# Kernel optimization log

Hardware: AMD Instinct MI355X
Metric: run time of the kernel (lower is better)

The kernel has to match this reference:

```python
import jax, jax.numpy as jnp
import numpy as np

B, S, D, H = 2, 2048, 1024, 16
DK = D // H  # 64


def setup_inputs() -> dict:
    key = jax.random.key(0)
    ks = jax.random.split(key, 12)
    inp = {
        "q": jax.random.normal(ks[0], (B, S, D), jnp.float32),
        "k": jax.random.normal(ks[1], (B, S, D), jnp.float32),
        "v": jax.random.normal(ks[2], (B, S, D), jnp.float32),
        "mask": jax.random.randint(ks[3], (B, S, S), 0, 2).astype(bool),
        "prior_info": jax.random.normal(ks[4], (B, S, S), jnp.float32),
        # per-head q/k projections stacked [H, D, DK]; shared v projection [D, DK]
        "Wq": jax.random.normal(ks[5], (H, D, DK), jnp.float32) * 0.02,
        "bq": jnp.zeros((H, DK), jnp.float32),
        "Wk": jax.random.normal(ks[6], (H, D, DK), jnp.float32) * 0.02,
        "bk": jnp.zeros((H, DK), jnp.float32),
        "Wv": jax.random.normal(ks[7], (D, DK), jnp.float32) * 0.02,
        "bv": jnp.zeros((DK,), jnp.float32),
        "Wh": jax.random.normal(ks[8], (DK, D), jnp.float32) * 0.02,  # w_h, no bias
    }
    return inp


def reference(q, k, v, mask, prior_info, Wq, bq, Wk, bk, Wv, bv, Wh):
    NEG = jnp.asarray(-1e9, q.dtype)
    vs = v @ Wv + bv                                      # [B,S,DK] shared across heads
    qs = jnp.einsum("bsd,hdk->bhsk", q, Wq) + bq[None, :, None, :]
    ksh = jnp.einsum("btd,hdk->bhtk", k, Wk) + bk[None, :, None, :]
    scores = jnp.einsum("bhsk,bhtk->bhst", qs, ksh) / jnp.sqrt(
        jnp.asarray(DK, q.dtype))                         # [B,H,S,S]
    m = mask[:, None]                                     # [B,1,S,S]
    scores = jnp.where(m, NEG, scores)
    prior = jnp.where(m, NEG, prior_info[:, None])        # [B,1,S,S] -> broadcast
    z = jax.nn.sigmoid(scores + prior)
    blended = z * scores + (1 - z) * prior
    attn = jax.nn.softmax(blended, axis=-1)               # [B,H,S,S]
    heads = jnp.einsum("bhst,btk->bhsk", attn, vs)        # [B,H,S,DK]
    out = heads.mean(axis=1) @ Wh                          # [B,S,D]
    attn_out = jnp.transpose(attn, (0, 2, 1, 3))           # torch stacks heads at dim=2
    return out, attn_out
```

## Files before the change

kernel.cpp:

```cpp
#include <hip/hip_runtime.h>

#define DEV __device__ __forceinline__

using f32x4  = __attribute__((ext_vector_type(4))) float;
using bf16x8 = __attribute__((ext_vector_type(8))) __bf16;
using u16x4  = __attribute__((ext_vector_type(4))) unsigned short;

constexpr int S_ = 2048, D_ = 1024, H_ = 16, DK_ = 64;
constexpr float LOG2E_ = 1.44269504f;
constexpr float M2_ = 8.0f * 1.44269504f;
constexpr float C1_ = 0.125f * 1.44269504f;

DEV unsigned short f2bf(float x) {
  unsigned int u = __float_as_uint(x);
  u += 0x7fffu + ((u >> 16) & 1u);
  return (unsigned short)(u >> 16);
}

DEV float bf2f(unsigned short u) {
  return __uint_as_float((unsigned int)u << 16);
}

DEV void gload_lds16(const void* g, void* l) {
  __builtin_amdgcn_global_load_lds(
      (__attribute__((address_space(1))) void*)g,
      (__attribute__((address_space(3))) void*)l, 16, 0, 0);
}

DEV f32x4 mfma_bf16(bf16x8 a, bf16x8 b, f32x4 c) {
  return __builtin_amdgcn_mfma_f32_16x16x32_bf16(a, b, c, 0, 0, 0);
}


__global__ __launch_bounds__(256) void qkv_to_bf16(
    const float* __restrict__ q, const float* __restrict__ k,
    const float* __restrict__ v, unsigned short* __restrict__ dst) {
  int seg = blockIdx.x >> 12;
  int j = ((blockIdx.x & 4095) << 8) + threadIdx.x;
  const float* s = seg == 0 ? q : (seg == 1 ? k : v);
  unsigned short* d = dst + (size_t)seg * 4194304;
  f32x4 val = *(const f32x4*)(s + (size_t)j * 4);
  u16x4 o;
  o[0] = f2bf(val[0]); o[1] = f2bf(val[1]); o[2] = f2bf(val[2]); o[3] = f2bf(val[3]);
  *(u16x4*)(d + (size_t)j * 4) = o;
}

__global__ __launch_bounds__(256) void make_pm2(
    const int* __restrict__ mask, const float* __restrict__ prior,
    unsigned short* __restrict__ pm2, int n4) {
  int i = blockIdx.x * 256 + threadIdx.x;
  if (i >= n4) return;
  const int* m = mask + (size_t)i * 4;
  f32x4 p = *(const f32x4*)(prior + (size_t)i * 4);
  u16x4 o;
#pragma unroll
  for (int j = 0; j < 4; ++j)
    o[j] = f2bf(m[j] ? -1.44269504e9f : p[j] * LOG2E_);
  *(u16x4*)(pm2 + (size_t)i * 4) = o;
}

__global__ __launch_bounds__(256) void pack_wqk2(
    const float* __restrict__ Wq, const float* __restrict__ Wk,
    unsigned short* __restrict__ WT) {
  int seg = blockIdx.x >> 12;
  int i = ((blockIdx.x & 4095) << 8) + threadIdx.x;
  const float* W = seg ? Wk : Wq;
  int d = i & 1023, n = i >> 10;
  int hh = n >> 6, kk = n & 63;
  WT[(size_t)seg * 1048576 + i] = f2bf(W[((size_t)hh * 1024 + d) * 64 + kk]);
}

__global__ __launch_bounds__(256) void pack_wv(
    const float* __restrict__ W, unsigned short* __restrict__ WT) {
  int i = blockIdx.x * 256 + threadIdx.x;
  int d = i & 1023, kk = i >> 10;
  WT[i] = f2bf(W[(size_t)d * 64 + kk]);
}

__global__ __launch_bounds__(256) void pack_wh(
    const float* __restrict__ W, unsigned short* __restrict__ WT) {
  int i = blockIdx.x * 256 + threadIdx.x;
  int k = i & 63, n = i >> 6;
  WT[i] = f2bf(W[(size_t)k * 1024 + n]);
}

__global__ __launch_bounds__(256) void mean_heads(
    const float* __restrict__ hp, unsigned short* __restrict__ hbar) {
  int i = blockIdx.x * 256 + threadIdx.x;
  int kk = i & 63, m = i >> 6;
  int b = m >> 11, s = m & 2047;
  float acc = 0.f;
#pragma unroll
  for (int hh = 0; hh < 16; ++hh)
    acc += hp[(((size_t)b * 16 + hh) * 2048 + s) * 64 + kk];
  hbar[i] = f2bf(acc * 0.0625f);
}


template <int BN, int MODE>
__global__ __launch_bounds__(256) void gemm_bt(
    const unsigned short* __restrict__ A, const unsigned short* __restrict__ BT,
    const float* __restrict__ bias, void* __restrict__ outp, int M, int N, int K) {
  constexpr int BM = 128, BK = 64;
  constexpr int NWC = BN / 64;
  constexpr int NWR = 4 / NWC;
  constexpr int WTM = BM / NWR;
  constexpr int MI = WTM / 16;
  constexpr int NI = 4;
  __shared__ unsigned short ldsA[BM * BK];
  __shared__ unsigned short ldsB[BN * BK];
  const int tid = threadIdx.x;
  const int wave = tid >> 6, lane = tid & 63;
  const int g = lane >> 4, l4 = lane & 15;
  const int m0 = blockIdx.x * BM, n0 = blockIdx.y * BN;
  const int wr = wave / NWC, wc = wave % NWC;
  const int r8 = lane >> 3, s8 = lane & 7;
  f32x4 acc[MI][NI];
#pragma unroll
  for (int mi = 0; mi < MI; ++mi)
#pragma unroll
    for (int ni = 0; ni < NI; ++ni) acc[mi][ni] = {0.f, 0.f, 0.f, 0.f};

  for (int k0 = 0; k0 < K; k0 += BK) {
    __syncthreads();
#pragma unroll
    for (int j = 0; j < 4; ++j) {
      int c = wave * 4 + j;
      int row = c * 8 + r8;
      int slot = s8 ^ (row & 7);
      gload_lds16(A + (size_t)(m0 + row) * K + k0 + slot * 8, &ldsA[c * 512]);
    }
    constexpr int BCH = BN * BK / 512;
#pragma unroll
    for (int j = 0; j < BCH / 4; ++j) {
      int c = wave * (BCH / 4) + j;
      int row = c * 8 + r8;
      int slot = s8 ^ (row & 7);
      gload_lds16(BT + (size_t)(n0 + row) * K + k0 + slot * 8, &ldsB[c * 512]);
    }
    __syncthreads();
    bf16x8 af[MI][2], bfr[NI][2];
#pragma unroll
    for (int mi = 0; mi < MI; ++mi)
#pragma unroll
      for (int kss = 0; kss < 2; ++kss) {
        int row = wr * WTM + mi * 16 + l4;
        int slot = (kss * 4 + g) ^ (row & 7);
        af[mi][kss] = *(const bf16x8*)&ldsA[row * 64 + slot * 8];
      }
#pragma unroll
    for (int ni = 0; ni < NI; ++ni)
#pragma unroll
      for (int kss = 0; kss < 2; ++kss) {
        int row = wc * 64 + ni * 16 + l4;
        int slot = (kss * 4 + g) ^ (row & 7);
        bfr[ni][kss] = *(const bf16x8*)&ldsB[row * 64 + slot * 8];
      }
#pragma unroll
    for (int mi = 0; mi < MI; ++mi)
#pragma unroll
      for (int ni = 0; ni < NI; ++ni)
#pragma unroll
        for (int kss = 0; kss < 2; ++kss)
          acc[mi][ni] = mfma_bf16(af[mi][kss], bfr[ni][kss], acc[mi][ni]);
  }

#pragma unroll
  for (int mi = 0; mi < MI; ++mi)
#pragma unroll
    for (int ni = 0; ni < NI; ++ni)
#pragma unroll
      for (int r = 0; r < 4; ++r) {
        int m = m0 + wr * WTM + mi * 16 + g * 4 + r;
        int n = n0 + wc * 64 + ni * 16 + l4;
        float c = acc[mi][ni][r];
        if constexpr (MODE != 2) c += bias[n];
        if constexpr (MODE == 0) {
          int b = m >> 11, s = m & 2047, hh = n >> 6, kk = n & 63;
          ((unsigned short*)outp)[(((size_t)b * 16 + hh) * 2048 + s) * 64 + kk] = f2bf(c);
        } else if constexpr (MODE == 1) {
          int b = m >> 11, t = m & 2047;
          ((unsigned short*)outp)[((size_t)b * 64 + n) * 2048 + t] = f2bf(c);
        } else {
          ((float*)outp)[(size_t)m * N + n] = c;
        }
      }
}


__global__ __launch_bounds__(512, 2) void attn_fused1(
    const unsigned short* __restrict__ qs, const unsigned short* __restrict__ ks,
    const unsigned short* __restrict__ vsT, const unsigned short* __restrict__ pm2,
    float* __restrict__ attn_out, float* __restrict__ heads) {
  __shared__ unsigned short lds_p[8][32 * 256];
  __shared__ float lds_sum[8][32];

  const int tid = threadIdx.x;
  const int w = tid >> 6, lane = tid & 63;
  const int g = lane >> 4, l4 = lane & 15;
  const int blk = ((blockIdx.x & 7) << 8) + (blockIdx.x >> 3);
  const int sblk = blk & 63, bh = blk >> 6;
  const int b = bh >> 4, h = bh & 15;
  const int tb = w << 8;

  const unsigned short* qsb = qs + ((size_t)bh * S_ + sblk * 32) * DK_;
  const unsigned short* ksb = ks + (size_t)bh * S_ * DK_ + (size_t)tb * DK_;
  const unsigned short* pmrow0 = pm2 + ((size_t)b * S_ + sblk * 32 + l4) * S_ + tb;
  const unsigned short* pmrow1 = pmrow0 + (size_t)16 * S_;
  const unsigned short* vtb = vsT + (size_t)b * DK_ * S_ + tb;

  bf16x8 aq0[2], aq1[2];
#pragma unroll
  for (int kss = 0; kss < 2; ++kss) {
    aq0[kss] = *(const bf16x8*)(qsb + (size_t)l4 * DK_ + (kss * 4 + g) * 8);
    aq1[kss] = *(const bf16x8*)(qsb + (size_t)(16 + l4) * DK_ + (kss * 4 + g) * 8);
  }

  char* pbase = (char*)&lds_p[w][0];
  const int swz = (l4 & 7) << 4;

  float lsum0 = 0.f, lsum1 = 0.f;
  u16x4 pc0[2][4], pc1[2][4];
#pragma unroll
  for (int d = 0; d < 2; ++d)
#pragma unroll
    for (int ct = 0; ct < 4; ++ct) {
      pc0[d][ct] = *(const u16x4*)(pmrow0 + d * 64 + ct * 16 + g * 4);
      pc1[d][ct] = *(const u16x4*)(pmrow1 + d * 64 + ct * 16 + g * 4);
    }
  bf16x8 kf[2][4][2];
#pragma unroll
  for (int ct = 0; ct < 4; ++ct)
#pragma unroll
    for (int kss = 0; kss < 2; ++kss)
      kf[0][ct][kss] = *(const bf16x8*)(ksb +
          (size_t)(ct * 16 + l4) * DK_ + (kss * 4 + g) * 8);

#pragma unroll
  for (int i = 0; i < 4; ++i) {
    const int tr = i * 64;
    const int cur = i & 1, nxt = (i + 1) & 1;
    if (i + 1 < 4) {
#pragma unroll
      for (int ct = 0; ct < 4; ++ct)
#pragma unroll
        for (int kss = 0; kss < 2; ++kss)
          kf[nxt][ct][kss] = *(const bf16x8*)(ksb +
              (size_t)((i + 1) * 64 + ct * 16 + l4) * DK_ + (kss * 4 + g) * 8);
    }
#pragma unroll
    for (int ct = 0; ct < 4; ++ct) {
      f32x4 a0 = {0.f, 0.f, 0.f, 0.f}, a1 = {0.f, 0.f, 0.f, 0.f};
#pragma unroll
      for (int kss = 0; kss < 2; ++kss) {
        a0 = mfma_bf16(kf[cur][ct][kss], aq0[kss], a0);
        a1 = mfma_bf16(kf[cur][ct][kss], aq1[kss], a1);
      }
      u16x4 pb0, pb1;
#pragma unroll
      for (int r = 0; r < 4; ++r) {
        {
          float pmv = bf2f(pc0[cur][ct][r]);
          float sc2 = a0[r] * C1_;
          float e = __builtin_amdgcn_exp2f(-(sc2 + pmv));
          float z = __builtin_amdgcn_rcpf(1.f + e);
          float p = __builtin_amdgcn_exp2f(pmv + z * (sc2 - pmv) - M2_);
          lsum0 += p;
          pb0[r] = f2bf(p);
        }
        {
          float pmv = bf2f(pc1[cur][ct][r]);
          float sc2 = a1[r] * C1_;
          float e = __builtin_amdgcn_exp2f(-(sc2 + pmv));
          float z = __builtin_amdgcn_rcpf(1.f + e);
          float p = __builtin_amdgcn_exp2f(pmv + z * (sc2 - pmv) - M2_);
          lsum1 += p;
          pb1[r] = f2bf(p);
        }
      }
      const int toff = ((tr + ct * 16 + g * 4) * 2) ^ swz;
      *(u16x4*)(pbase + (size_t)l4 * 512 + toff) = pb0;
      *(u16x4*)(pbase + (size_t)(16 + l4) * 512 + toff) = pb1;
    }
    if (i + 2 < 4) {
#pragma unroll
      for (int ct = 0; ct < 4; ++ct) {
        pc0[cur][ct] = *(const u16x4*)(pmrow0 + (i + 2) * 64 + ct * 16 + g * 4);
        pc1[cur][ct] = *(const u16x4*)(pmrow1 + (i + 2) * 64 + ct * 16 + g * 4);
      }
    }
  }
  lsum0 += __shfl_xor(lsum0, 16);
  lsum0 += __shfl_xor(lsum0, 32);
  lsum1 += __shfl_xor(lsum1, 16);
  lsum1 += __shfl_xor(lsum1, 32);
  if (g == 0) {
    lds_sum[w][l4] = lsum0;
    lds_sum[w][16 + l4] = lsum1;
  }

  __syncthreads();

  float invl0, invl1;
  {
    float s0 = 0.f, s1 = 0.f;
#pragma unroll
    for (int wv = 0; wv < 8; ++wv) {
      s0 += lds_sum[wv][l4];
      s1 += lds_sum[wv][16 + l4];
    }
    invl0 = 1.f / s0;
    invl1 = 1.f / s1;
  }

  f32x4 acc0_[4], acc1_[4];
#pragma unroll
  for (int ni = 0; ni < 4; ++ni) {
    acc0_[ni] = {0.f, 0.f, 0.f, 0.f};
    acc1_[ni] = {0.f, 0.f, 0.f, 0.f};
  }

  float* attrow0 = attn_out +
      (((size_t)b * S_ + sblk * 32 + l4) * H_ + h) * S_ + tb;
  float* attrow1 = attrow0 + (size_t)16 * H_ * S_;

  bf16x8 vf[2][4];
#pragma unroll
  for (int ni = 0; ni < 4; ++ni)
    vf[0][ni] = *(const bf16x8*)(vtb + (size_t)(ni * 16 + l4) * S_ + g * 8);

#pragma unroll
  for (int st = 0; st < 8; ++st) {
    const int t0 = st * 32;
    const int cur = st & 1, nxt = (st + 1) & 1;
    if (st + 1 < 8) {
#pragma unroll
      for (int ni = 0; ni < 4; ++ni)
        vf[nxt][ni] = *(const bf16x8*)(vtb +
            (size_t)(ni * 16 + l4) * S_ + t0 + 32 + g * 8);
    }
    const int toff = ((t0 + g * 8) * 2) ^ swz;
    bf16x8 pa0 = *(const bf16x8*)(pbase + (size_t)l4 * 512 + toff);
    bf16x8 pa1 = *(const bf16x8*)(pbase + (size_t)(16 + l4) * 512 + toff);
    f32x4 a0, a1, a2, a3;
#pragma unroll
    for (int j = 0; j < 4; ++j) {
      a0[j] = (float)pa0[j] * invl0;
      a1[j] = (float)pa0[4 + j] * invl0;
      a2[j] = (float)pa1[j] * invl1;
      a3[j] = (float)pa1[4 + j] * invl1;
    }
    *(f32x4*)(attrow0 + t0 + g * 8) = a0;
    *(f32x4*)(attrow0 + t0 + g * 8 + 4) = a1;
    *(f32x4*)(attrow1 + t0 + g * 8) = a2;
    *(f32x4*)(attrow1 + t0 + g * 8 + 4) = a3;
#pragma unroll
    for (int ni = 0; ni < 4; ++ni) {
      acc0_[ni] = mfma_bf16(pa0, vf[cur][ni], acc0_[ni]);
      acc1_[ni] = mfma_bf16(pa1, vf[cur][ni], acc1_[ni]);
    }
  }

  float* pr_lds = (float*)pbase;
#pragma unroll
  for (int ni = 0; ni < 4; ++ni)
#pragma unroll
    for (int r = 0; r < 4; ++r) {
      pr_lds[(g * 4 + r) * 64 + ni * 16 + l4] = acc0_[ni][r];
      pr_lds[(16 + g * 4 + r) * 64 + ni * 16 + l4] = acc1_[ni][r];
    }

  __syncthreads();

  {
    int row = tid >> 4;
    float sv = 0.f;
#pragma unroll
    for (int wv = 0; wv < 8; ++wv) sv += lds_sum[wv][row];
    float iv = 1.f / sv;
    f32x4 s4 = {0.f, 0.f, 0.f, 0.f};
#pragma unroll
    for (int wv = 0; wv < 8; ++wv) {
      f32x4 part = *(const f32x4*)((char*)&lds_p[wv][0] + tid * 16);
      s4[0] += part[0]; s4[1] += part[1]; s4[2] += part[2]; s4[3] += part[3];
    }
    s4[0] *= iv; s4[1] *= iv; s4[2] *= iv; s4[3] *= iv;
    *(f32x4*)(heads + ((size_t)bh * S_ + sblk * 32) * 64 + tid * 4) = s4;
  }
}


extern "C" void kernel_launch(void* const* d_in, const int* in_sizes, int n_in,
                              void* d_out, int out_size, void* d_ws, size_t ws_size,
                              hipStream_t stream) {
  (void)in_sizes; (void)n_in; (void)out_size; (void)ws_size;
  const float* q     = (const float*)d_in[0];
  const float* k     = (const float*)d_in[1];
  const float* v     = (const float*)d_in[2];
  const int*   mask  = (const int*)d_in[3];
  const float* prior = (const float*)d_in[4];
  const float* Wq    = (const float*)d_in[5];
  const float* bq    = (const float*)d_in[6];
  const float* Wk    = (const float*)d_in[7];
  const float* bk    = (const float*)d_in[8];
  const float* Wv    = (const float*)d_in[9];
  const float* bv    = (const float*)d_in[10];
  const float* Wh    = (const float*)d_in[11];

  float* out  = (float*)d_out;
  float* attn = out + (size_t)4096 * 1024;

  char* ws = (char*)d_ws;
  unsigned short* q_bf  = (unsigned short*)(ws + 0);
  unsigned short* pm2   = (unsigned short*)(ws + 0);
  float*          heads = (float*)(ws + 33554432);
  unsigned short* WqT   = (unsigned short*)(ws + 50331648);
  unsigned short* WvT   = (unsigned short*)(ws + 54525952);
  unsigned short* WhT   = (unsigned short*)(ws + 54657024);
  unsigned short* qs_bf = (unsigned short*)(ws + 54788096);
  unsigned short* ks_bf = (unsigned short*)(ws + 63176704);
  unsigned short* vsT   = (unsigned short*)(ws + 71565312);
  unsigned short* hbar  = (unsigned short*)(ws + 72089600);

  qkv_to_bf16<<<12288, 256, 0, stream>>>(q, k, v, q_bf);
  pack_wqk2<<<8192, 256, 0, stream>>>(Wq, Wk, WqT);
  pack_wv<<<256, 256, 0, stream>>>(Wv, WvT);
  pack_wh<<<256, 256, 0, stream>>>(Wh, WhT);

  gemm_bt<128, 0><<<dim3(32, 8), 256, 0, stream>>>(q_bf, WqT, bq, qs_bf, 4096, 1024, 1024);
  gemm_bt<128, 0><<<dim3(32, 8), 256, 0, stream>>>(q_bf + 4194304, WqT + 1048576, bk, ks_bf, 4096, 1024, 1024);
  gemm_bt<64, 1><<<dim3(32, 1), 256, 0, stream>>>(q_bf + 8388608, WvT, bv, vsT, 4096, 64, 1024);

  make_pm2<<<8192, 256, 0, stream>>>(mask, prior, pm2, 2097152);

  attn_fused1<<<2048, 512, 0, stream>>>(qs_bf, ks_bf, vsT, pm2, attn, heads);

  mean_heads<<<1024, 256, 0, stream>>>(heads, hbar);
  gemm_bt<128, 2><<<dim3(32, 8), 256, 0, stream>>>(hbar, WhT, nullptr, out, 4096, 1024, 64);
}
```

Measured before the change: 410.1 us.

## Pre-swizzle prior/mask tensor into per-wave fragment order and regroup heads per block

```diff
diff --git a/kernel.cpp b/kernel.cpp
--- a/kernel.cpp
+++ b/kernel.cpp
@@ -3,6 +3,7 @@
 #define DEV __device__ __forceinline__
 
 using f32x4  = __attribute__((ext_vector_type(4))) float;
+using int4v  = __attribute__((ext_vector_type(4))) int;
 using bf16x8 = __attribute__((ext_vector_type(8))) __bf16;
 using u16x4  = __attribute__((ext_vector_type(4))) unsigned short;
 
@@ -45,18 +46,24 @@
   *(u16x4*)(d + (size_t)j * 4) = o;
 }
 
-__global__ __launch_bounds__(256) void make_pm2(
+__global__ __launch_bounds__(256) void make_pm3(
     const int* __restrict__ mask, const float* __restrict__ prior,
-    unsigned short* __restrict__ pm2, int n4) {
-  int i = blockIdx.x * 256 + threadIdx.x;
-  if (i >= n4) return;
-  const int* m = mask + (size_t)i * 4;
-  f32x4 p = *(const f32x4*)(prior + (size_t)i * 4);
+    unsigned short* __restrict__ pm3) {
+  int tid = blockIdx.x * 256 + threadIdx.x;
+  int lane = tid & 63, cidx = tid >> 6;
+  int rs = cidx & 1, ct = (cidx >> 1) & 3, i = (cidx >> 3) & 3;
+  int w = (cidx >> 5) & 7, sblk = (cidx >> 8) & 63, b = cidx >> 14;
+  int g = lane >> 4, l4 = lane & 15;
+  int s = sblk * 32 + rs * 16 + l4;
+  int t = w * 256 + i * 64 + ct * 16 + g * 4;
+  size_t off = ((size_t)b * S_ + s) * S_ + t;
+  int4v m = *(const int4v*)(mask + off);
+  f32x4 p = *(const f32x4*)(prior + off);
   u16x4 o;
 #pragma unroll
   for (int j = 0; j < 4; ++j)
     o[j] = f2bf(m[j] ? -1.44269504e9f : p[j] * LOG2E_);
-  *(u16x4*)(pm2 + (size_t)i * 4) = o;
+  *(u16x4*)(pm3 + (size_t)tid * 4) = o;
 }
 
 __global__ __launch_bounds__(256) void pack_wqk2(
@@ -190,7 +197,7 @@
 
 __global__ __launch_bounds__(512, 2) void attn_fused1(
     const unsigned short* __restrict__ qs, const unsigned short* __restrict__ ks,
-    const unsigned short* __restrict__ vsT, const unsigned short* __restrict__ pm2,
+    const unsigned short* __restrict__ vsT, const unsigned short* __restrict__ pm3,
     float* __restrict__ attn_out, float* __restrict__ heads) {
   __shared__ unsigned short lds_p[8][32 * 256];
   __shared__ float lds_sum[8][32];
@@ -199,14 +206,16 @@
   const int w = tid >> 6, lane = tid & 63;
   const int g = lane >> 4, l4 = lane & 15;
   const int blk = ((blockIdx.x & 7) << 8) + (blockIdx.x >> 3);
-  const int sblk = blk & 63, bh = blk >> 6;
-  const int b = bh >> 4, h = bh & 15;
+  const int b = blk >> 10;
+  const int h = ((blk >> 9) & 1) * 8 + (blk & 7);
+  const int sblk = (blk >> 3) & 63;
+  const int bh = b * 16 + h;
   const int tb = w << 8;
 
   const unsigned short* qsb = qs + ((size_t)bh * S_ + sblk * 32) * DK_;
   const unsigned short* ksb = ks + (size_t)bh * S_ * DK_ + (size_t)tb * DK_;
-  const unsigned short* pmrow0 = pm2 + ((size_t)b * S_ + sblk * 32 + l4) * S_ + tb;
-  const unsigned short* pmrow1 = pmrow0 + (size_t)16 * S_;
+  const unsigned short* pmw = pm3 +
+      ((size_t)((b * 64 + sblk) * 8 + w) * 32) * 256;
   const unsigned short* vtb = vsT + (size_t)b * DK_ * S_ + tb;
 
   bf16x8 aq0[2], aq1[2];
@@ -225,8 +234,8 @@
   for (int d = 0; d < 2; ++d)
 #pragma unroll
     for (int ct = 0; ct < 4; ++ct) {
-      pc0[d][ct] = *(const u16x4*)(pmrow0 + d * 64 + ct * 16 + g * 4);
-      pc1[d][ct] = *(const u16x4*)(pmrow1 + d * 64 + ct * 16 + g * 4);
+      pc0[d][ct] = *(const u16x4*)(pmw + (size_t)((d * 4 + ct) * 2 + 0) * 256 + lane * 4);
+      pc1[d][ct] = *(const u16x4*)(pmw + (size_t)((d * 4 + ct) * 2 + 1) * 256 + lane * 4);
     }
   bf16x8 kf[2][4][2];
 #pragma unroll
@@ -285,8 +294,8 @@
     if (i + 2 < 4) {
 #pragma unroll
       for (int ct = 0; ct < 4; ++ct) {
-        pc0[cur][ct] = *(const u16x4*)(pmrow0 + (i + 2) * 64 + ct * 16 + g * 4);
-        pc1[cur][ct] = *(const u16x4*)(pmrow1 + (i + 2) * 64 + ct * 16 + g * 4);
+        pc0[cur][ct] = *(const u16x4*)(pmw + (size_t)(((i + 2) * 4 + ct) * 2 + 0) * 256 + lane * 4);
+        pc1[cur][ct] = *(const u16x4*)(pmw + (size_t)(((i + 2) * 4 + ct) * 2 + 1) * 256 + lane * 4);
       }
     }
   }
@@ -412,7 +421,7 @@
 
   char* ws = (char*)d_ws;
   unsigned short* q_bf  = (unsigned short*)(ws + 0);
-  unsigned short* pm2   = (unsigned short*)(ws + 0);
+  unsigned short* pm3   = (unsigned short*)(ws + 0);
   float*          heads = (float*)(ws + 33554432);
   unsigned short* WqT   = (unsigned short*)(ws + 50331648);
   unsigned short* WvT   = (unsigned short*)(ws + 54525952);
@@ -431,9 +440,9 @@
   gemm_bt<128, 0><<<dim3(32, 8), 256, 0, stream>>>(q_bf + 4194304, WqT + 1048576, bk, ks_bf, 4096, 1024, 1024);
   gemm_bt<64, 1><<<dim3(32, 1), 256, 0, stream>>>(q_bf + 8388608, WvT, bv, vsT, 4096, 64, 1024);
 
-  make_pm2<<<8192, 256, 0, stream>>>(mask, prior, pm2, 2097152);
-
-  attn_fused1<<<2048, 512, 0, stream>>>(qs_bf, ks_bf, vsT, pm2, attn, heads);
+  make_pm3<<<8192, 256, 0, stream>>>(mask, prior, pm3);
+
+  attn_fused1<<<2048, 512, 0, stream>>>(qs_bf, ks_bf, vsT, pm3, attn, heads);
 
   mean_heads<<<1024, 256, 0, stream>>>(heads, hbar);
   gemm_bt<128, 2><<<dim3(32, 8), 256, 0, stream>>>(hbar, WhT, nullptr, out, 4096, 1024, 64);
```

Measured after the change: 373.2 us. 1.1x faster.
